# Optimization experiments

Measured on AMD Instinct MI355X. Metric: run time of the kernel, lower is better.

## Reference

```python
import jax, jax.numpy as jnp
import numpy as np

B, T, IN, H, L, C = 64, 2048, 64, 128, 2, 8


def setup_inputs() -> dict:
    key = jax.random.key(0)
    ks = jax.random.split(key, 11)
    s = 1.0 / np.sqrt(H)  # torch nn.RNN default init scale
    return {
        "x": jax.random.normal(ks[0], (B, T, IN), dtype=jnp.float32),
        "W_ih0": jax.random.uniform(ks[1], (H, IN), jnp.float32, -s, s),
        "W_hh0": jax.random.uniform(ks[2], (H, H), jnp.float32, -s, s),
        "b_ih0": jax.random.uniform(ks[3], (H,), jnp.float32, -s, s),
        "b_hh0": jax.random.uniform(ks[4], (H,), jnp.float32, -s, s),
        "W_ih1": jax.random.uniform(ks[5], (H, H), jnp.float32, -s, s),
        "W_hh1": jax.random.uniform(ks[6], (H, H), jnp.float32, -s, s),
        "b_ih1": jax.random.uniform(ks[7], (H,), jnp.float32, -s, s),
        "b_hh1": jax.random.uniform(ks[8], (H,), jnp.float32, -s, s),
        "W_fc": jax.random.uniform(ks[9], (C, H), jnp.float32, -s, s),
        "b_fc": jax.random.uniform(ks[10], (C,), jnp.float32, -s, s),
    }


def _rnn_layer(x, W_ih, W_hh, b_ih, b_hh):
    # x: (B, T, D_in) -> (B, T, H); h0 = zeros (matches torch h0)
    # Precompute the input projection as one big GEMM outside the scan.
    x_proj = jnp.einsum('btd,hd->bth', x, W_ih) + b_ih + b_hh  # (B,T,H)
    x_proj_t = jnp.swapaxes(x_proj, 0, 1)  # (T,B,H)
    h0 = jnp.zeros((x.shape[0], W_hh.shape[0]), dtype=x.dtype)

    def step(h, xp):
        h_new = jnp.tanh(xp + h @ W_hh.T)
        return h_new, h_new

    _, hs = jax.lax.scan(step, h0, x_proj_t)  # (T,B,H)
    return jnp.swapaxes(hs, 0, 1)  # (B,T,H)


def reference(x, W_ih0, W_hh0, b_ih0, b_hh0, W_ih1, W_hh1, b_ih1, b_hh1, W_fc, b_fc):
    h1 = _rnn_layer(x, W_ih0, W_hh0, b_ih0, b_hh0)   # layer 0
    h2 = _rnn_layer(h1, W_ih1, W_hh1, b_ih1, b_hh1)  # layer 1
    logits = jnp.einsum('bth,ch->btc', h2, W_fc) + b_fc  # (B,T,C)
    return logits
```

## Files before the change

kernel.cpp:

```cpp
#include <hip/hip_runtime.h>

#define B_ 64
#define T_ 2048
#define IN_ 64
#define H_ 128
#define C_ 8

__device__ __forceinline__ float tanh_fast(float x) {
  float e = __expf(2.0f * x);
  return 1.0f - 2.0f * __builtin_amdgcn_rcpf(e + 1.0f);
}

__device__ __forceinline__ void fma4(float4& a, const float4 w, const float4 h) {
  a.x = fmaf(w.x, h.x, a.x);
  a.y = fmaf(w.y, h.y, a.y);
  a.z = fmaf(w.z, h.z, a.z);
  a.w = fmaf(w.w, h.w, a.w);
}
__device__ __forceinline__ float hsum4(const float4 a) { return (a.x + a.y) + (a.z + a.w); }

__device__ __forceinline__ float dpp_add_x1(float v) {
  return v + __int_as_float(__builtin_amdgcn_update_dpp(0, __float_as_int(v), 0xB1, 0xF, 0xF, true));
}
__device__ __forceinline__ float dpp_add_x2(float v) {
  return v + __int_as_float(__builtin_amdgcn_update_dpp(0, __float_as_int(v), 0x4E, 0xF, 0xF, true));
}
__device__ __forceinline__ float swz_add_x4(float v) {
  return v + __int_as_float(__builtin_amdgcn_ds_swizzle(__float_as_int(v), 0x101F));
}

__device__ __forceinline__ void block_sync_lds() {
  asm volatile("s_waitcnt lgkmcnt(0)" ::: "memory");
  __builtin_amdgcn_s_barrier();
  asm volatile("" ::: "memory");
}

__global__ __launch_bounds__(256) void k_xproj0(
    const float* __restrict__ x,
    const float* __restrict__ Wih0,
    const float* __restrict__ bih0,
    const float* __restrict__ bhh0,
    float* __restrict__ xp0) {
  __shared__ __align__(16) float xs[4][IN_];
  const int wave = threadIdx.x >> 6;
  const int lane = threadIdx.x & 63;
  const int gw   = blockIdx.x * 4 + wave;
  const int rows = (B_ * T_) / 2048;
  const int r0   = gw * rows;

  float4 w0[16], w1[16];
  const float4* W4 = (const float4*)Wih0;
#pragma unroll
  for (int k = 0; k < 16; ++k) {
    w0[k] = W4[lane * 16 + k];
    w1[k] = W4[(lane + 64) * 16 + k];
  }
  const float ba = bih0[lane] + bhh0[lane];
  const float bb = bih0[lane + 64] + bhh0[lane + 64];

  float xnext = x[(size_t)r0 * IN_ + lane];
  for (int rr = 0; rr < rows; ++rr) {
    const int r = r0 + rr;
    xs[wave][lane] = xnext;
    if (rr + 1 < rows) xnext = x[(size_t)(r + 1) * IN_ + lane];
    asm volatile("s_waitcnt lgkmcnt(0)" ::: "memory");
    float4 a0 = {0.f, 0.f, 0.f, 0.f}, a1 = {0.f, 0.f, 0.f, 0.f};
    const float4* xv = (const float4*)xs[wave];
#pragma unroll
    for (int k = 0; k < 16; ++k) {
      float4 h = xv[k];
      fma4(a0, w0[k], h);
      fma4(a1, w1[k], h);
    }
    xp0[(size_t)r * H_ + lane]      = hsum4(a0) + ba;
    xp0[(size_t)r * H_ + 64 + lane] = hsum4(a1) + bb;
  }
}

#define L0STEP(SS, XA, XB)                                               \
  {                                                                      \
    block_sync_lds();                                                    \
    const int s_ = (SS);                                                 \
    if (s_ < T_) {                                                       \
      const float4* hp = (const float4*)h1r[(s_ + 1) & 1];               \
      float4 a0 = {0.f,0.f,0.f,0.f}, a1 = {0.f,0.f,0.f,0.f};             \
      _Pragma("unroll")                                                  \
      for (int k4 = 0; k4 < 8; ++k4) {                                   \
        float4 hv = hp[kq * 8 + ((k4 + 2 * kq) & 7)];                    \
        fma4(a0, wa[k4], hv);                                            \
        fma4(a1, wb[k4], hv);                                            \
      }                                                                  \
      float t0 = dpp_add_x2(dpp_add_x1(hsum4(a0)));                      \
      float t1 = dpp_add_x2(dpp_add_x1(hsum4(a1)));                      \
      if (kq == 0) {                                                     \
        h1r[s_ & 1][j]      = tanh_fast(t0 + XA);                        \
        h1r[s_ & 1][j + 64] = tanh_fast(t1 + XB);                        \
        const int sp = s_ + 4;                                           \
        if (sp < T_) {                                                   \
          XA = xp0[xpb + (size_t)sp * H_ + j];                           \
          XB = xp0[xpb + (size_t)sp * H_ + j + 64];                      \
        }                                                                \
      }                                                                  \
    }                                                                    \
  }

__global__ __launch_bounds__(832) void k_rnn(
    const float* __restrict__ xp0,
    const float* __restrict__ Whh0,
    const float* __restrict__ Wih1,
    const float* __restrict__ Whh1,
    const float* __restrict__ bih1,
    const float* __restrict__ bhh1,
    const float* __restrict__ Wfc,
    const float* __restrict__ bfc,
    float* __restrict__ out) {
  __shared__ __align__(16) float h1r[2][H_];
  __shared__ __align__(16) float h2r[2][H_];

  const int tid  = threadIdx.x;
  const int wave = tid >> 6;
  const int lane = tid & 63;
  const int b    = blockIdx.x;

  if (tid < 2 * H_) {
    ((float*)h1r)[tid] = 0.f;
    ((float*)h2r)[tid] = 0.f;
  }
  block_sync_lds();

  if (wave < 4) {
    const int jj = lane >> 2;
    const int kq = lane & 3;
    const int j  = wave * 16 + jj;
    const float4* W4 = (const float4*)Whh0;
    float4 wa[8], wb[8];
#pragma unroll
    for (int k4 = 0; k4 < 8; ++k4) {
      const int m = (k4 + 2 * kq) & 7;
      wa[k4] = W4[j * 32 + kq * 8 + m];
      wb[k4] = W4[(j + 64) * 32 + kq * 8 + m];
    }
    const size_t xpb = (size_t)b * T_ * H_;
    float XA0 = 0.f, XA1 = 0.f, XA2 = 0.f, XA3 = 0.f;
    float XB0 = 0.f, XB1 = 0.f, XB2 = 0.f, XB3 = 0.f;
    if (kq == 0) {
      XA0 = xp0[xpb + 0 * H_ + j]; XB0 = xp0[xpb + 0 * H_ + j + 64];
      XA1 = xp0[xpb + 1 * H_ + j]; XB1 = xp0[xpb + 1 * H_ + j + 64];
      XA2 = xp0[xpb + 2 * H_ + j]; XB2 = xp0[xpb + 2 * H_ + j + 64];
      XA3 = xp0[xpb + 3 * H_ + j]; XB3 = xp0[xpb + 3 * H_ + j + 64];
    }
    for (int s0 = 0; s0 < T_ + 4; s0 += 4) {
      L0STEP(s0 + 0, XA0, XB0);
      L0STEP(s0 + 1, XA1, XB1);
      L0STEP(s0 + 2, XA2, XB2);
      L0STEP(s0 + 3, XA3, XB3);
    }
  } else if (wave < 12) {
    const int w1 = wave - 4;
    const int jj = lane >> 3;
    const int ke = lane & 7;
    const int j  = w1 * 8 + jj;
    const int kq = ke & 3;
    const float4* W4 = (const float4*)((ke < 4) ? Wih1 : Whh1);
    float4 va[8], vb[8];
#pragma unroll
    for (int k4 = 0; k4 < 8; ++k4) {
      const int m = (k4 + ke) & 7;
      va[k4] = W4[j * 32 + kq * 8 + m];
      vb[k4] = W4[(j + 64) * 32 + kq * 8 + m];
    }
    const float bA = bih1[j] + bhh1[j];
    const float bB = bih1[j + 64] + bhh1[j + 64];
    for (int s = 0; s < T_ + 4; ++s) {
      block_sync_lds();
      if (s >= 1 && s <= T_) {
        const float* hbase = (ke < 4) ? h1r[(s + 1) & 1]
                                      : h2r[s & 1];
        const float4* hp = (const float4*)hbase;
        float4 a0 = {0.f,0.f,0.f,0.f}, a1 = {0.f,0.f,0.f,0.f};
#pragma unroll
        for (int k4 = 0; k4 < 8; ++k4) {
          float4 hv = hp[kq * 8 + ((k4 + ke) & 7)];
          fma4(a0, va[k4], hv);
          fma4(a1, vb[k4], hv);
        }
        float t0 = swz_add_x4(dpp_add_x2(dpp_add_x1(hsum4(a0))));
        float t1 = swz_add_x4(dpp_add_x2(dpp_add_x1(hsum4(a1))));
        if (ke == 0) {
          h2r[(s + 1) & 1][j]      = tanh_fast(t0 + bA);
          h2r[(s + 1) & 1][j + 64] = tanh_fast(t1 + bB);
        }
      }
    }
  } else {
    const int c   = lane >> 3;
    const int seg = lane & 7;
    const float4* W4 = (const float4*)Wfc;
    float4 wf[4];
#pragma unroll
    for (int k4 = 0; k4 < 4; ++k4) wf[k4] = W4[c * 32 + seg * 4 + k4];
    const float bv = bfc[c];
    float* outb = out + (size_t)b * T_ * C_;
    for (int s = 0; s < T_ + 4; ++s) {
      block_sync_lds();
      if (s >= 2 && s < T_ + 2) {
        const float4* hp = (const float4*)h2r[s & 1];
        float4 a = {0.f,0.f,0.f,0.f};
#pragma unroll
        for (int k4 = 0; k4 < 4; ++k4) fma4(a, wf[k4], hp[seg * 4 + k4]);
        float t = swz_add_x4(dpp_add_x2(dpp_add_x1(hsum4(a))));
        if (seg == 0) outb[(size_t)(s - 2) * C_ + c] = t + bv;
      }
    }
  }
}

extern "C" void kernel_launch(void* const* d_in, const int* in_sizes, int n_in,
                              void* d_out, int out_size, void* d_ws, size_t ws_size,
                              hipStream_t stream) {
  const float* x    = (const float*)d_in[0];
  const float* Wih0 = (const float*)d_in[1];
  const float* Whh0 = (const float*)d_in[2];
  const float* bih0 = (const float*)d_in[3];
  const float* bhh0 = (const float*)d_in[4];
  const float* Wih1 = (const float*)d_in[5];
  const float* Whh1 = (const float*)d_in[6];
  const float* bih1 = (const float*)d_in[7];
  const float* bhh1 = (const float*)d_in[8];
  const float* Wfc  = (const float*)d_in[9];
  const float* bfc  = (const float*)d_in[10];
  float* outp = (float*)d_out;
  float* xp0  = (float*)d_ws;

  k_xproj0<<<512, 256, 0, stream>>>(x, Wih0, bih0, bhh0, xp0);
  k_rnn<<<64, 832, 0, stream>>>(xp0, Whh0, Wih1, Whh1, bih1, bhh1, Wfc, bfc, outp);
}
```

Before: 1.238 ms.

## Switch recurrent matvecs and projections to fp16 packed dot2 with fp32 accumulate

Converts the weights and the LDS hidden-state buffers to packed fp16 and replaces the fp32 FMA chains with v_dot2_f32_f16, which halves the FMA instruction count and LDS read volume on the serial per-timestep critical path. It also stores the layer-0 input projection as fp16 to halve workspace traffic, and reorganises the LDS layout and thread-to-output mapping so each lane produces two adjacent outputs. In exchange, fp16 rounding of the weights, hidden states and projections may add enough error over 2048 recurrent steps to fail tolerance.

```diff
diff --git a/kernel.cpp b/kernel.cpp
--- a/kernel.cpp
+++ b/kernel.cpp
@@ -6,18 +6,27 @@
 #define H_ 128
 #define C_ 8
 
+typedef _Float16 f16x2 __attribute__((ext_vector_type(2)));
+
+__device__ __forceinline__ f16x2 pk(float a, float b) {
+  f16x2 r; r.x = (_Float16)a; r.y = (_Float16)b; return r;
+}
+__device__ __forceinline__ f16x2 as_h2(int v) { return __builtin_bit_cast(f16x2, v); }
+
+__device__ __forceinline__ float dot2(f16x2 a, f16x2 b, float c) {
+#if __has_builtin(__builtin_amdgcn_fdot2)
+  return __builtin_amdgcn_fdot2(a, b, c, false);
+#else
+  float r;
+  asm("v_dot2_f32_f16 %0, %1, %2, %3" : "=v"(r) : "v"(a), "v"(b), "v"(c));
+  return r;
+#endif
+}
+
 __device__ __forceinline__ float tanh_fast(float x) {
   float e = __expf(2.0f * x);
   return 1.0f - 2.0f * __builtin_amdgcn_rcpf(e + 1.0f);
 }
-
-__device__ __forceinline__ void fma4(float4& a, const float4 w, const float4 h) {
-  a.x = fmaf(w.x, h.x, a.x);
-  a.y = fmaf(w.y, h.y, a.y);
-  a.z = fmaf(w.z, h.z, a.z);
-  a.w = fmaf(w.w, h.w, a.w);
-}
-__device__ __forceinline__ float hsum4(const float4 a) { return (a.x + a.y) + (a.z + a.w); }
 
 __device__ __forceinline__ float dpp_add_x1(float v) {
   return v + __int_as_float(__builtin_amdgcn_update_dpp(0, __float_as_int(v), 0xB1, 0xF, 0xF, true));
@@ -35,77 +44,113 @@
   asm volatile("" ::: "memory");
 }
 
-__global__ __launch_bounds__(256) void k_xproj0(
-    const float* __restrict__ x,
-    const float* __restrict__ Wih0,
-    const float* __restrict__ bih0,
-    const float* __restrict__ bhh0,
-    float* __restrict__ xp0) {
-  __shared__ __align__(16) float xs[4][IN_];
-  const int wave = threadIdx.x >> 6;
-  const int lane = threadIdx.x & 63;
-  const int gw   = blockIdx.x * 4 + wave;
-  const int rows = (B_ * T_) / 2048;
-  const int r0   = gw * rows;
-
-  float4 w0[16], w1[16];
-  const float4* W4 = (const float4*)Wih0;
-#pragma unroll
-  for (int k = 0; k < 16; ++k) {
-    w0[k] = W4[lane * 16 + k];
-    w1[k] = W4[(lane + 64) * 16 + k];
-  }
-  const float ba = bih0[lane] + bhh0[lane];
-  const float bb = bih0[lane + 64] + bhh0[lane + 64];
-
-  float xnext = x[(size_t)r0 * IN_ + lane];
-  for (int rr = 0; rr < rows; ++rr) {
-    const int r = r0 + rr;
-    xs[wave][lane] = xnext;
-    if (rr + 1 < rows) xnext = x[(size_t)(r + 1) * IN_ + lane];
+#define DOT8(A, Q, W, BASE)            \
+  A = dot2(as_h2(Q.x), W[BASE+0], A);  \
+  A = dot2(as_h2(Q.y), W[BASE+1], A);  \
+  A = dot2(as_h2(Q.z), W[BASE+2], A);  \
+  A = dot2(as_h2(Q.w), W[BASE+3], A);
+
+__global__ __launch_bounds__(256) void k_xproj(
+    const float* __restrict__ x, const float* __restrict__ Wih0,
+    const float* __restrict__ bih0, const float* __restrict__ bhh0,
+    _Float16* __restrict__ xp) {
+  __shared__ __align__(16) _Float16 xs[4][2][IN_];
+  const int wave = threadIdx.x >> 6, lane = threadIdx.x & 63;
+  const int gw = blockIdx.x * 4 + wave;
+  const int ROWS = 32;
+  const size_t r0 = (size_t)gw * ROWS;
+
+  f16x2 wA[32], wB[32];
+  const float2* W2 = (const float2*)Wih0;
+#pragma unroll
+  for (int p = 0; p < 32; ++p) {
+    float2 a = W2[(lane * 2) * 32 + p];
+    float2 b = W2[(lane * 2 + 1) * 32 + p];
+    wA[p] = pk(a.x, a.y); wB[p] = pk(b.x, b.y);
+  }
+  const float ba = bih0[lane * 2] + bhh0[lane * 2];
+  const float bb = bih0[lane * 2 + 1] + bhh0[lane * 2 + 1];
+
+  xs[wave][0][lane] = (_Float16)x[r0 * IN_ + lane];
+  float xn = x[(r0 + 1) * IN_ + lane];
+  for (int rr = 0; rr < ROWS; ++rr) {
+    const int buf = rr & 1;
+    if (rr + 1 < ROWS) xs[wave][buf ^ 1][lane] = (_Float16)xn;
+    if (rr + 2 < ROWS) xn = x[(r0 + rr + 2) * IN_ + lane];
     asm volatile("s_waitcnt lgkmcnt(0)" ::: "memory");
-    float4 a0 = {0.f, 0.f, 0.f, 0.f}, a1 = {0.f, 0.f, 0.f, 0.f};
-    const float4* xv = (const float4*)xs[wave];
-#pragma unroll
-    for (int k = 0; k < 16; ++k) {
-      float4 h = xv[k];
-      fma4(a0, w0[k], h);
-      fma4(a1, w1[k], h);
-    }
-    xp0[(size_t)r * H_ + lane]      = hsum4(a0) + ba;
-    xp0[(size_t)r * H_ + 64 + lane] = hsum4(a1) + bb;
-  }
-}
-
-#define L0STEP(SS, XA, XB)                                               \
-  {                                                                      \
-    block_sync_lds();                                                    \
-    const int s_ = (SS);                                                 \
-    if (s_ < T_) {                                                       \
-      const float4* hp = (const float4*)h1r[(s_ + 1) & 1];               \
-      float4 a0 = {0.f,0.f,0.f,0.f}, a1 = {0.f,0.f,0.f,0.f};             \
-      _Pragma("unroll")                                                  \
-      for (int k4 = 0; k4 < 8; ++k4) {                                   \
-        float4 hv = hp[kq * 8 + ((k4 + 2 * kq) & 7)];                    \
-        fma4(a0, wa[k4], hv);                                            \
-        fma4(a1, wb[k4], hv);                                            \
-      }                                                                  \
-      float t0 = dpp_add_x2(dpp_add_x1(hsum4(a0)));                      \
-      float t1 = dpp_add_x2(dpp_add_x1(hsum4(a1)));                      \
-      if (kq == 0) {                                                     \
-        h1r[s_ & 1][j]      = tanh_fast(t0 + XA);                        \
-        h1r[s_ & 1][j + 64] = tanh_fast(t1 + XB);                        \
-        const int sp = s_ + 4;                                           \
-        if (sp < T_) {                                                   \
-          XA = xp0[xpb + (size_t)sp * H_ + j];                           \
-          XB = xp0[xpb + (size_t)sp * H_ + j + 64];                      \
-        }                                                                \
-      }                                                                  \
-    }                                                                    \
+    const int4* xv = (const int4*)xs[wave][buf];
+    int4 q0 = xv[0], q1 = xv[1], q2 = xv[2], q3 = xv[3];
+    int4 q4 = xv[4], q5 = xv[5], q6 = xv[6], q7 = xv[7];
+    float a0 = 0.f, a1 = 0.f, c0 = 0.f, c1 = 0.f;
+    DOT8(a0, q0, wA, 0)  DOT8(c0, q0, wB, 0)
+    DOT8(a1, q1, wA, 4)  DOT8(c1, q1, wB, 4)
+    DOT8(a0, q2, wA, 8)  DOT8(c0, q2, wB, 8)
+    DOT8(a1, q3, wA, 12) DOT8(c1, q3, wB, 12)
+    DOT8(a0, q4, wA, 16) DOT8(c0, q4, wB, 16)
+    DOT8(a1, q5, wA, 20) DOT8(c1, q5, wB, 20)
+    DOT8(a0, q6, wA, 24) DOT8(c0, q6, wB, 24)
+    DOT8(a1, q7, wA, 28) DOT8(c1, q7, wB, 28)
+    *(f16x2*)&xp[(r0 + rr) * H_ + lane * 2] = pk(a0 + a1 + ba, c0 + c1 + bb);
+  }
+}
+
+#define L0STEP(SS, XA, RI, WI)                                             \
+  {                                                                        \
+    block_sync_lds();                                                      \
+    const int s_ = (SS);                                                   \
+    if (s_ < T_) {                                                         \
+      int4 q0 = hp[(RI) + rot0], q1 = hp[(RI) + rot1];                     \
+      int4 q2 = hp[(RI) + rot2], q3 = hp[(RI) + rot3];                     \
+      float a0 = 0.f, a1 = 0.f, c0 = 0.f, c1 = 0.f;                        \
+      DOT8(a0, q0, wA, 0)  DOT8(c0, q0, wB, 0)                             \
+      DOT8(a1, q1, wA, 4)  DOT8(c1, q1, wB, 4)                             \
+      DOT8(a0, q2, wA, 8)  DOT8(c0, q2, wB, 8)                             \
+      DOT8(a1, q3, wA, 12) DOT8(c1, q3, wB, 12)                            \
+      float ra = dpp_add_x2(dpp_add_x1(a0 + a1));                          \
+      float rc = dpp_add_x2(dpp_add_x1(c0 + c1));                          \
+      float t0 = tanh_fast(ra + (float)XA.x);                              \
+      float t1 = tanh_fast(rc + (float)XA.y);                              \
+      const int sp = s_ + 4;                                               \
+      if (sp < T_) XA = xp2[xpb + (size_t)sp * 64 + jx];                   \
+      if (kq == 0) wp[(WI)] = pk(t0, t1);                                  \
+    }                                                                      \
+  }
+
+#define L1STEP(SS, RI, WI)                                                 \
+  {                                                                        \
+    block_sync_lds();                                                      \
+    const int s_ = (SS);                                                   \
+    if (s_ >= 1 && s_ <= T_) {                                             \
+      int4 q0 = hp[(RI) + rot0], q1 = hp[(RI) + rot1];                     \
+      int4 q2 = hp[(RI) + rot2], q3 = hp[(RI) + rot3];                     \
+      float a0 = 0.f, a1 = 0.f, c0 = 0.f, c1 = 0.f;                        \
+      DOT8(a0, q0, vA, 0)  DOT8(c0, q0, vB, 0)                             \
+      DOT8(a1, q1, vA, 4)  DOT8(c1, q1, vB, 4)                             \
+      DOT8(a0, q2, vA, 8)  DOT8(c0, q2, vB, 8)                             \
+      DOT8(a1, q3, vA, 12) DOT8(c1, q3, vB, 12)                            \
+      float ra = swz_add_x4(dpp_add_x2(dpp_add_x1(a0 + a1)));              \
+      float rc = swz_add_x4(dpp_add_x2(dpp_add_x1(c0 + c1)));              \
+      float t0 = tanh_fast(ra + bA);                                       \
+      float t1 = tanh_fast(rc + bB);                                       \
+      if (ke == 0) wp[(WI)] = pk(t0, t1);                                  \
+    }                                                                      \
+  }
+
+#define FCSTEP(SS, RI)                                                     \
+  {                                                                        \
+    block_sync_lds();                                                      \
+    const int s_ = (SS);                                                   \
+    if (s_ >= 2 && s_ < T_ + 2) {                                          \
+      int4 q0 = hp[(RI)], q1 = hp[(RI) + 1];                               \
+      float a0 = 0.f, a1 = 0.f;                                            \
+      DOT8(a0, q0, wf, 0) DOT8(a1, q1, wf, 4)                              \
+      float r = swz_add_x4(dpp_add_x2(dpp_add_x1(a0 + a1)));               \
+      if (k8 == 0) outb[(size_t)(s_ - 2) * C_ + c] = r + bv;               \
+    }                                                                      \
   }
 
 __global__ __launch_bounds__(832) void k_rnn(
-    const float* __restrict__ xp0,
+    const _Float16* __restrict__ xp0,
     const float* __restrict__ Whh0,
     const float* __restrict__ Wih1,
     const float* __restrict__ Whh1,
@@ -114,103 +159,90 @@
     const float* __restrict__ Wfc,
     const float* __restrict__ bfc,
     float* __restrict__ out) {
-  __shared__ __align__(16) float h1r[2][H_];
-  __shared__ __align__(16) float h2r[2][H_];
+  __shared__ __align__(16) _Float16 hlds[4][H_];
 
   const int tid  = threadIdx.x;
   const int wave = tid >> 6;
   const int lane = tid & 63;
   const int b    = blockIdx.x;
 
-  if (tid < 2 * H_) {
-    ((float*)h1r)[tid] = 0.f;
-    ((float*)h2r)[tid] = 0.f;
-  }
+  if (tid < 256) ((int*)hlds)[tid] = 0;
+  const int4*  hp = (const int4*)hlds;
+  f16x2*       wp = (f16x2*)hlds;
   block_sync_lds();
 
   if (wave < 4) {
-    const int jj = lane >> 2;
-    const int kq = lane & 3;
-    const int j  = wave * 16 + jj;
-    const float4* W4 = (const float4*)Whh0;
-    float4 wa[8], wb[8];
-#pragma unroll
-    for (int k4 = 0; k4 < 8; ++k4) {
-      const int m = (k4 + 2 * kq) & 7;
-      wa[k4] = W4[j * 32 + kq * 8 + m];
-      wb[k4] = W4[(j + 64) * 32 + kq * 8 + m];
-    }
-    const size_t xpb = (size_t)b * T_ * H_;
-    float XA0 = 0.f, XA1 = 0.f, XA2 = 0.f, XA3 = 0.f;
-    float XB0 = 0.f, XB1 = 0.f, XB2 = 0.f, XB3 = 0.f;
-    if (kq == 0) {
-      XA0 = xp0[xpb + 0 * H_ + j]; XB0 = xp0[xpb + 0 * H_ + j + 64];
-      XA1 = xp0[xpb + 1 * H_ + j]; XB1 = xp0[xpb + 1 * H_ + j + 64];
-      XA2 = xp0[xpb + 2 * H_ + j]; XB2 = xp0[xpb + 2 * H_ + j + 64];
-      XA3 = xp0[xpb + 3 * H_ + j]; XB3 = xp0[xpb + 3 * H_ + j + 64];
-    }
+    const int jj = lane >> 2, kq = lane & 3;
+    const int j0 = wave * 32 + jj * 2;
+    const int rot0 = kq, rot1 = (1 + kq) & 3, rot2 = (2 + kq) & 3, rot3 = (3 + kq) & 3;
+    f16x2 wA[16], wB[16];
+    const float2* W2 = (const float2*)Whh0;
+#pragma unroll
+    for (int m = 0; m < 4; ++m) {
+      const int cb = kq * 16 + (((m + kq) & 3)) * 4;
+#pragma unroll
+      for (int p = 0; p < 4; ++p) {
+        float2 a = W2[j0 * 64 + cb + p];
+        float2 bt = W2[(j0 + 1) * 64 + cb + p];
+        wA[m * 4 + p] = pk(a.x, a.y);
+        wB[m * 4 + p] = pk(bt.x, bt.y);
+      }
+    }
+    const int riE = 16 + kq * 4, riO = kq * 4;
+    const int wiE = (j0 >> 1), wiO = 64 + (j0 >> 1);
+    const size_t xpb = (size_t)b * T_ * 64;
+    const int jx = wave * 16 + jj;
+    const f16x2* xp2 = (const f16x2*)xp0;
+    f16x2 XA0 = xp2[xpb + 0 * 64 + jx], XA1 = xp2[xpb + 1 * 64 + jx];
+    f16x2 XA2 = xp2[xpb + 2 * 64 + jx], XA3 = xp2[xpb + 3 * 64 + jx];
     for (int s0 = 0; s0 < T_ + 4; s0 += 4) {
-      L0STEP(s0 + 0, XA0, XB0);
-      L0STEP(s0 + 1, XA1, XB1);
-      L0STEP(s0 + 2, XA2, XB2);
-      L0STEP(s0 + 3, XA3, XB3);
+      L0STEP(s0 + 0, XA0, riE, wiE)
+      L0STEP(s0 + 1, XA1, riO, wiO)
+      L0STEP(s0 + 2, XA2, riE, wiE)
+      L0STEP(s0 + 3, XA3, riO, wiO)
     }
   } else if (wave < 12) {
-    const int w1 = wave - 4;
-    const int jj = lane >> 3;
-    const int ke = lane & 7;
-    const int j  = w1 * 8 + jj;
-    const int kq = ke & 3;
-    const float4* W4 = (const float4*)((ke < 4) ? Wih1 : Whh1);
-    float4 va[8], vb[8];
-#pragma unroll
-    for (int k4 = 0; k4 < 8; ++k4) {
-      const int m = (k4 + ke) & 7;
-      va[k4] = W4[j * 32 + kq * 8 + m];
-      vb[k4] = W4[(j + 64) * 32 + kq * 8 + m];
-    }
-    const float bA = bih1[j] + bhh1[j];
-    const float bB = bih1[j + 64] + bhh1[j + 64];
-    for (int s = 0; s < T_ + 4; ++s) {
-      block_sync_lds();
-      if (s >= 1 && s <= T_) {
-        const float* hbase = (ke < 4) ? h1r[(s + 1) & 1]
-                                      : h2r[s & 1];
-        const float4* hp = (const float4*)hbase;
-        float4 a0 = {0.f,0.f,0.f,0.f}, a1 = {0.f,0.f,0.f,0.f};
-#pragma unroll
-        for (int k4 = 0; k4 < 8; ++k4) {
-          float4 hv = hp[kq * 8 + ((k4 + ke) & 7)];
-          fma4(a0, va[k4], hv);
-          fma4(a1, vb[k4], hv);
-        }
-        float t0 = swz_add_x4(dpp_add_x2(dpp_add_x1(hsum4(a0))));
-        float t1 = swz_add_x4(dpp_add_x2(dpp_add_x1(hsum4(a1))));
-        if (ke == 0) {
-          h2r[(s + 1) & 1][j]      = tanh_fast(t0 + bA);
-          h2r[(s + 1) & 1][j + 64] = tanh_fast(t1 + bB);
-        }
+    const int u = wave - 4;
+    const int jj = lane >> 3, ke = lane & 7, kq = ke & 3;
+    const int j0 = u * 16 + jj * 2;
+    const int rot0 = kq, rot1 = (1 + kq) & 3, rot2 = (2 + kq) & 3, rot3 = (3 + kq) & 3;
+    f16x2 vA[16], vB[16];
+    const float2* W2 = (const float2*)(ke < 4 ? Wih1 : Whh1);
+#pragma unroll
+    for (int m = 0; m < 4; ++m) {
+      const int cb = kq * 16 + (((m + kq) & 3)) * 4;
+#pragma unroll
+      for (int p = 0; p < 4; ++p) {
+        float2 a = W2[j0 * 64 + cb + p];
+        float2 bt = W2[(j0 + 1) * 64 + cb + p];
+        vA[m * 4 + p] = pk(a.x, a.y);
+        vB[m * 4 + p] = pk(bt.x, bt.y);
       }
     }
+    const float bA = bih1[j0] + bhh1[j0];
+    const float bB = bih1[j0 + 1] + bhh1[j0 + 1];
+    const int riE = (ke < 4 ? 16 : 32) + kq * 4;
+    const int riO = (ke < 4 ? 0 : 48) + kq * 4;
+    const int wiE = 192 + (j0 >> 1), wiO = 128 + (j0 >> 1);
+    for (int s = 0; s < T_ + 4; s += 2) {
+      L1STEP(s,     riE, wiE)
+      L1STEP(s + 1, riO, wiO)
+    }
   } else {
-    const int c   = lane >> 3;
-    const int seg = lane & 7;
-    const float4* W4 = (const float4*)Wfc;
-    float4 wf[4];
-#pragma unroll
-    for (int k4 = 0; k4 < 4; ++k4) wf[k4] = W4[c * 32 + seg * 4 + k4];
+    const int c = lane >> 3, k8 = lane & 7;
+    f16x2 wf[8];
+    const float2* W2 = (const float2*)Wfc;
+#pragma unroll
+    for (int p = 0; p < 8; ++p) {
+      float2 a = W2[c * 64 + k8 * 8 + p];
+      wf[p] = pk(a.x, a.y);
+    }
     const float bv = bfc[c];
     float* outb = out + (size_t)b * T_ * C_;
-    for (int s = 0; s < T_ + 4; ++s) {
-      block_sync_lds();
-      if (s >= 2 && s < T_ + 2) {
-        const float4* hp = (const float4*)h2r[s & 1];
-        float4 a = {0.f,0.f,0.f,0.f};
-#pragma unroll
-        for (int k4 = 0; k4 < 4; ++k4) fma4(a, wf[k4], hp[seg * 4 + k4]);
-        float t = swz_add_x4(dpp_add_x2(dpp_add_x1(hsum4(a))));
-        if (seg == 0) outb[(size_t)(s - 2) * C_ + c] = t + bv;
-      }
+    const int riE = 32 + k8 * 2, riO = 48 + k8 * 2;
+    for (int s = 0; s < T_ + 4; s += 2) {
+      FCSTEP(s,     riE)
+      FCSTEP(s + 1, riO)
     }
   }
 }
@@ -230,8 +262,8 @@
   const float* Wfc  = (const float*)d_in[9];
   const float* bfc  = (const float*)d_in[10];
   float* outp = (float*)d_out;
-  float* xp0  = (float*)d_ws;
-
-  k_xproj0<<<512, 256, 0, stream>>>(x, Wih0, bih0, bhh0, xp0);
+  _Float16* xp0 = (_Float16*)d_ws;
+
+  k_xproj<<<1024, 256, 0, stream>>>(x, Wih0, bih0, bhh0, xp0);
   k_rnn<<<64, 832, 0, stream>>>(xp0, Whh0, Wih1, Whh1, bih1, bhh1, Wfc, bfc, outp);
 }
```

After: 1.104 ms. 1.12x faster.
